# Kernel optimization log

Hardware: AMD Instinct MI355X
Metric: run time of the kernel (lower is better)

The kernel has to match this reference:

```python
import jax, jax.numpy as jnp
import numpy as np

B = 32768          # batch (replay-buffer minibatch)
OBS, ACT = 17, 6   # HalfCheetah-style dims
IN = OBS + ACT
H = 256            # hidden width hard-coded in the module
N = 10             # num_q_nets


def setup_inputs() -> dict:
    key = jax.random.key(0)
    ks = jax.random.split(key, 8)
    # PyTorch Linear default init: U(-1/sqrt(fan_in), 1/sqrt(fan_in)); scale randn similarly.
    s1, s2, s3 = 1.0 / np.sqrt(IN), 1.0 / np.sqrt(H), 1.0 / np.sqrt(H)
    return {
        "state": jax.random.normal(ks[0], (B, OBS), dtype=jnp.float32),
        "action": jax.random.uniform(ks[1], (B, ACT), dtype=jnp.float32, minval=-1.0, maxval=1.0),
        "W1": jax.random.normal(ks[2], (N, IN, H), dtype=jnp.float32) * s1,
        "b1": jax.random.normal(ks[3], (N, H), dtype=jnp.float32) * s1,
        "W2": jax.random.normal(ks[4], (N, H, H), dtype=jnp.float32) * s2,
        "b2": jax.random.normal(ks[5], (N, H), dtype=jnp.float32) * s2,
        "W3": jax.random.normal(ks[6], (N, H, 1), dtype=jnp.float32) * s3,
        "b3": jax.random.normal(ks[7], (N, 1), dtype=jnp.float32) * s3,
    }


def reference(state, action, W1, b1, W2, b2, W3, b3):
    # x: [B, OBS+ACT]
    x = jnp.concatenate([state, action], axis=1)
    # batched-over-ensemble GEMMs; n=ensemble member, b=batch
    h1 = jax.nn.relu(jnp.einsum("bi,nih->nbh", x, W1) + b1[:, None, :])   # [N,B,H]
    h2 = jax.nn.relu(jnp.einsum("nbh,nho->nbo", h1, W2) + b2[:, None, :])  # [N,B,H]
    out = jnp.einsum("nbh,nho->nbo", h2, W3) + b3[:, None, :]              # [N,B,1]
    return out
```

## Files before the change

kernel.cpp:

```cpp
#include <hip/hip_runtime.h>
#include <hip/hip_bf16.h>


typedef __attribute__((ext_vector_type(8))) short bf16x8;
typedef __attribute__((ext_vector_type(4))) float f32x4;

#define B_TOTAL 32768
#define NQ 10
#define HDIM 256
#define BT 64

#define W1P_ELEMS (NQ * 16 * 64 * 8)
#define W2P_ELEMS (NQ * 8 * 16 * 64 * 8)

__device__ __forceinline__ unsigned short f2bf(float f) {
  unsigned int u = __float_as_uint(f);
  u = u + 0x7FFFu + ((u >> 16) & 1u);
  return (unsigned short)(u >> 16);
}

__device__ __forceinline__ unsigned int pk2bf(float a, float b) {
  union { __hip_bfloat162 h; unsigned int u; } cv;
  cv.h = __float22bfloat162_rn(make_float2(a, b));
  return cv.u;
}

__global__ void pack_w_kernel(const float* __restrict__ W1,
                              const float* __restrict__ W2,
                              unsigned short* __restrict__ w1p,
                              unsigned short* __restrict__ w2p) {
  int t = blockIdx.x * 256 + threadIdx.x;
  const int NW1 = NQ * 16 * 64;
  if (t < NW1) {
    int u = t;
    int lane = u & 63, mt = (u >> 6) & 15, n = u >> 10;
    int m = lane & 15, q = lane >> 4;
    int outc = mt * 16 + m;
    unsigned short v[8];
#pragma unroll
    for (int j = 0; j < 8; j++) {
      int k = q * 8 + j;
      v[j] = (k < 23) ? f2bf(W1[(n * 23 + k) * 256 + outc]) : (unsigned short)0;
    }
    *(uint4*)&w1p[(size_t)u * 8] = *(const uint4*)v;
  } else {
    int u = t - NW1;
    int lane = u & 63, mt = (u >> 6) & 15, kt = (u >> 10) & 7, n = u >> 13;
    int m = lane & 15, q = lane >> 4;
    int outc = mt * 16 + m;
    unsigned short v[8];
#pragma unroll
    for (int j = 0; j < 8; j++) {
      int h = kt * 32 + q * 8 + j;
      v[j] = f2bf(W2[((size_t)(n * 256 + h)) * 256 + outc]);
    }
    *(uint4*)&w2p[(size_t)u * 8] = *(const uint4*)v;
  }
}

__global__ __launch_bounds__(256, 4) void fused_ensemble_kernel(
    const float* __restrict__ state,
    const float* __restrict__ action,
    const unsigned short* __restrict__ w1p,
    const float* __restrict__ b1,
    const unsigned short* __restrict__ w2p,
    const float* __restrict__ b2,
    const float* __restrict__ W3,
    const float* __restrict__ b3,
    float* __restrict__ out) {
  __shared__ __align__(16) unsigned short hs[32 * BT * 8];
  __shared__ __align__(16) unsigned short xs[BT * 32];
  __shared__ float red[4 * 64];

  const int tid = threadIdx.x;
  const int lane = tid & 63;
  const int w = tid >> 6;
  const int m = lane & 15;
  const int q = lane >> 4;

  const int n = blockIdx.x >> 9;
  const int row0 = (blockIdx.x & 511) * BT;

  f32x4 acc[4][4];

  bf16x8 af1[4];
#pragma unroll
  for (int mt = 0; mt < 4; mt++)
    af1[mt] = *(const bf16x8*)(w1p + (((size_t)n * 16 + w * 4 + mt) * 64 + lane) * 8);
  float4 b1v[4];
#pragma unroll
  for (int mt = 0; mt < 4; mt++)
    b1v[mt] = *(const float4*)&b1[n * HDIM + (w * 4 + mt) * 16 + q * 4];

  {
    int r = tid >> 2, seg = tid & 3;
    int row = row0 + r;
    unsigned short v[8];
    if (seg < 2) {
      const float* sp = state + (size_t)row * 17 + seg * 8;
#pragma unroll
      for (int j = 0; j < 8; j++) v[j] = f2bf(sp[j]);
    } else if (seg == 2) {
      v[0] = f2bf(state[(size_t)row * 17 + 16]);
      const float* ap = action + (size_t)row * 6;
#pragma unroll
      for (int j = 0; j < 6; j++) v[1 + j] = f2bf(ap[j]);
      v[7] = 0;
    } else {
#pragma unroll
      for (int j = 0; j < 8; j++) v[j] = 0;
    }
    *(uint4*)&xs[(size_t)r * 32 + seg * 8] = *(const uint4*)v;
  }
  __syncthreads();

  {
    bf16x8 bfr[4];
#pragma unroll
    for (int nt = 0; nt < 4; nt++)
      bfr[nt] = *(const bf16x8*)&xs[(size_t)(nt * 16 + m) * 32 + q * 8];
#pragma unroll
    for (int mt = 0; mt < 4; mt++) {
      float4 bv = b1v[mt];
      f32x4 bi = (f32x4){bv.x, bv.y, bv.z, bv.w};
#pragma unroll
      for (int nt = 0; nt < 4; nt++) acc[mt][nt] = bi;
    }
    __builtin_amdgcn_s_setprio(1);
#pragma unroll
    for (int nt = 0; nt < 4; nt++)
#pragma unroll
      for (int mt = 0; mt < 4; mt++)
        acc[mt][nt] = __builtin_amdgcn_mfma_f32_16x16x32_bf16(af1[mt], bfr[nt], acc[mt][nt], 0, 0, 0);
    __builtin_amdgcn_s_setprio(0);
  }

#pragma unroll
  for (int mt = 0; mt < 4; mt++) {
    int kq = w * 8 + mt * 2 + (q >> 1);
    int joff = (q & 1) * 4;
#pragma unroll
    for (int nt = 0; nt < 4; nt++) {
      int col = nt * 16 + m;
      f32x4 a = acc[mt][nt];
      uint2 wv;
      wv.x = pk2bf(fmaxf(a[0], 0.f), fmaxf(a[1], 0.f));
      wv.y = pk2bf(fmaxf(a[2], 0.f), fmaxf(a[3], 0.f));
      *(uint2*)&hs[((size_t)kq * BT + col) * 8 + joff] = wv;
    }
  }

  const unsigned short* w2n = w2p + (size_t)n * (8 * 16 * 64 * 8);
  bf16x8 acur[4], anxt[4];
#pragma unroll
  for (int mt = 0; mt < 4; mt++)
    acur[mt] = *(const bf16x8*)(w2n + (((size_t)w * 4 + mt) * 64 + lane) * 8);
  float4 b2v[4];
#pragma unroll
  for (int mt = 0; mt < 4; mt++)
    b2v[mt] = *(const float4*)&b2[n * HDIM + (w * 4 + mt) * 16 + q * 4];
  __syncthreads();

  {
#pragma unroll
    for (int mt = 0; mt < 4; mt++) {
      float4 bv = b2v[mt];
      f32x4 bi = (f32x4){bv.x, bv.y, bv.z, bv.w};
#pragma unroll
      for (int nt = 0; nt < 4; nt++) acc[mt][nt] = bi;
    }
#pragma unroll
    for (int kt = 0; kt < 8; kt++) {
      if (kt < 7) {
#pragma unroll
        for (int mt = 0; mt < 4; mt++)
          anxt[mt] = *(const bf16x8*)(w2n + (((size_t)(kt + 1) * 16 + w * 4 + mt) * 64 + lane) * 8);
      }
      bf16x8 bfr[4];
#pragma unroll
      for (int nt = 0; nt < 4; nt++)
        bfr[nt] = *(const bf16x8*)&hs[(((size_t)kt * 4 + q) * BT + nt * 16 + m) * 8];
      __builtin_amdgcn_s_setprio(1);
#pragma unroll
      for (int nt = 0; nt < 4; nt++)
#pragma unroll
        for (int mt = 0; mt < 4; mt++)
          acc[mt][nt] = __builtin_amdgcn_mfma_f32_16x16x32_bf16(acur[mt], bfr[nt], acc[mt][nt], 0, 0, 0);
      __builtin_amdgcn_s_setprio(0);
#pragma unroll
      for (int mt = 0; mt < 4; mt++) acur[mt] = anxt[mt];
    }
  }

  {
    float4 w3v[4];
#pragma unroll
    for (int mt = 0; mt < 4; mt++)
      w3v[mt] = *(const float4*)&W3[n * HDIM + (w * 4 + mt) * 16 + q * 4];
    float p[4];
#pragma unroll
    for (int nt = 0; nt < 4; nt++) {
      float s = 0.f;
#pragma unroll
      for (int mt = 0; mt < 4; mt++) {
        f32x4 a = acc[mt][nt];
        float4 wv = w3v[mt];
        s = fmaf(fmaxf(a[0], 0.f), wv.x, s);
        s = fmaf(fmaxf(a[1], 0.f), wv.y, s);
        s = fmaf(fmaxf(a[2], 0.f), wv.z, s);
        s = fmaf(fmaxf(a[3], 0.f), wv.w, s);
      }
      s += __shfl_xor(s, 16, 64);
      s += __shfl_xor(s, 32, 64);
      p[nt] = s;
    }
    if (q == 0) {
#pragma unroll
      for (int nt = 0; nt < 4; nt++) red[w * 64 + nt * 16 + m] = p[nt];
    }
    __syncthreads();
    if (tid < BT) {
      float s = b3[n];
#pragma unroll
      for (int c = 0; c < 4; c++) s += red[c * 64 + tid];
      out[(size_t)n * B_TOTAL + row0 + tid] = s;
    }
  }
}

extern "C" void kernel_launch(void* const* d_in, const int* in_sizes, int n_in,
                              void* d_out, int out_size, void* d_ws, size_t ws_size,
                              hipStream_t stream) {
  const float* state  = (const float*)d_in[0];
  const float* action = (const float*)d_in[1];
  const float* W1 = (const float*)d_in[2];
  const float* b1 = (const float*)d_in[3];
  const float* W2 = (const float*)d_in[4];
  const float* b2 = (const float*)d_in[5];
  const float* W3 = (const float*)d_in[6];
  const float* b3 = (const float*)d_in[7];
  float* out = (float*)d_out;

  unsigned short* w1p = (unsigned short*)d_ws;
  unsigned short* w2p = (unsigned short*)((char*)d_ws + (size_t)W1P_ELEMS * 2);

  pack_w_kernel<<<360, 256, 0, stream>>>(W1, W2, w1p, w2p);
  fused_ensemble_kernel<<<NQ * (B_TOTAL / BT), 256, 0, stream>>>(
      state, action, w1p, b1, w2p, b2, W3, b3, out);
}
```

Baseline: 119.7 us.

## Switch GEMMs to 32x32x16 MFMA tiles and fold b1 into W1 padding

Replaces the 16x16x32 bf16 MFMA tiling with 32x32x16 MFMA instructions, repacking W1/W2 fragments and the LDS layouts of the input and hidden activations to match the new operand layout. Layer-1 bias is folded into the weight matrix by putting b1 in the padded K slot and setting the matching input element to 1.0, so the bias load and accumulator init go away. The larger MFMA tile issues fewer instructions and reuses operands more per instruction. It also changes the accumulator register layout and the shuffle reduction, which could affect register pressure and occupancy.

```diff
diff --git a/kernel.cpp b/kernel.cpp
--- a/kernel.cpp
+++ b/kernel.cpp
@@ -3,15 +3,15 @@
 
 
 typedef __attribute__((ext_vector_type(8))) short bf16x8;
-typedef __attribute__((ext_vector_type(4))) float f32x4;
+typedef __attribute__((ext_vector_type(16))) float f32x16;
 
 #define B_TOTAL 32768
 #define NQ 10
 #define HDIM 256
 #define BT 64
 
-#define W1P_ELEMS (NQ * 16 * 64 * 8)
-#define W2P_ELEMS (NQ * 8 * 16 * 64 * 8)
+#define W1P_ELEMS (NQ * 2 * 8 * 64 * 8)
+#define W2P_ELEMS (NQ * 8 * 2 * 8 * 64 * 8)
 
 __device__ __forceinline__ unsigned short f2bf(float f) {
   unsigned int u = __float_as_uint(f);
@@ -26,34 +26,34 @@
 }
 
 __global__ void pack_w_kernel(const float* __restrict__ W1,
+                              const float* __restrict__ b1,
                               const float* __restrict__ W2,
                               unsigned short* __restrict__ w1p,
                               unsigned short* __restrict__ w2p) {
   int t = blockIdx.x * 256 + threadIdx.x;
-  const int NW1 = NQ * 16 * 64;
+  const int NW1 = NQ * 2 * 8 * 64;
   if (t < NW1) {
     int u = t;
-    int lane = u & 63, mt = (u >> 6) & 15, n = u >> 10;
-    int m = lane & 15, q = lane >> 4;
-    int outc = mt * 16 + m;
+    int lane = u & 63, mtile = (u >> 6) & 7, ks = (u >> 9) & 1, n = u >> 10;
+    int outc = mtile * 32 + (lane & 31);
+    int kbase = ks * 16 + (lane >> 5) * 8;
     unsigned short v[8];
 #pragma unroll
     for (int j = 0; j < 8; j++) {
-      int k = q * 8 + j;
-      v[j] = (k < 23) ? f2bf(W1[(n * 23 + k) * 256 + outc]) : (unsigned short)0;
+      int k = kbase + j;
+      v[j] = (k < 23) ? f2bf(W1[(n * 23 + k) * 256 + outc])
+           : (k == 23) ? f2bf(b1[n * 256 + outc]) : (unsigned short)0;
     }
     *(uint4*)&w1p[(size_t)u * 8] = *(const uint4*)v;
   } else {
     int u = t - NW1;
-    int lane = u & 63, mt = (u >> 6) & 15, kt = (u >> 10) & 7, n = u >> 13;
-    int m = lane & 15, q = lane >> 4;
-    int outc = mt * 16 + m;
+    int lane = u & 63, mtile = (u >> 6) & 7, ks = (u >> 9) & 1, kt = (u >> 10) & 7, n = u >> 13;
+    int outc = mtile * 32 + (lane & 31);
+    int kbase = kt * 32 + ks * 16 + (lane >> 5) * 8;
     unsigned short v[8];
 #pragma unroll
-    for (int j = 0; j < 8; j++) {
-      int h = kt * 32 + q * 8 + j;
-      v[j] = f2bf(W2[((size_t)(n * 256 + h)) * 256 + outc]);
-    }
+    for (int j = 0; j < 8; j++)
+      v[j] = f2bf(W2[((size_t)(n * 256 + kbase + j)) * 256 + outc]);
     *(uint4*)&w2p[(size_t)u * 8] = *(const uint4*)v;
   }
 }
@@ -62,35 +62,32 @@
     const float* __restrict__ state,
     const float* __restrict__ action,
     const unsigned short* __restrict__ w1p,
-    const float* __restrict__ b1,
     const unsigned short* __restrict__ w2p,
     const float* __restrict__ b2,
     const float* __restrict__ W3,
     const float* __restrict__ b3,
     float* __restrict__ out) {
-  __shared__ __align__(16) unsigned short hs[32 * BT * 8];
-  __shared__ __align__(16) unsigned short xs[BT * 32];
+  __shared__ __align__(16) unsigned short hs[32 * 64 * 8];
+  __shared__ __align__(16) unsigned short xs[4 * 64 * 8];
   __shared__ float red[4 * 64];
 
   const int tid = threadIdx.x;
   const int lane = tid & 63;
   const int w = tid >> 6;
-  const int m = lane & 15;
-  const int q = lane >> 4;
+  const int c = lane & 31;
+  const int hi = lane >> 5;
 
   const int n = blockIdx.x >> 9;
   const int row0 = (blockIdx.x & 511) * BT;
 
-  f32x4 acc[4][4];
-
-  bf16x8 af1[4];
-#pragma unroll
-  for (int mt = 0; mt < 4; mt++)
-    af1[mt] = *(const bf16x8*)(w1p + (((size_t)n * 16 + w * 4 + mt) * 64 + lane) * 8);
-  float4 b1v[4];
-#pragma unroll
-  for (int mt = 0; mt < 4; mt++)
-    b1v[mt] = *(const float4*)&b1[n * HDIM + (w * 4 + mt) * 16 + q * 4];
+  f32x16 acc[2][2];
+
+  bf16x8 af1[2][2];
+#pragma unroll
+  for (int ks = 0; ks < 2; ks++)
+#pragma unroll
+    for (int mt = 0; mt < 2; mt++)
+      af1[ks][mt] = *(const bf16x8*)(w1p + ((((size_t)n * 2 + ks) * 8 + w * 2 + mt) * 64 + lane) * 8);
 
   {
     int r = tid >> 2, seg = tid & 3;
@@ -105,124 +102,150 @@
       const float* ap = action + (size_t)row * 6;
 #pragma unroll
       for (int j = 0; j < 6; j++) v[1 + j] = f2bf(ap[j]);
-      v[7] = 0;
+      v[7] = 0x3F80;
     } else {
 #pragma unroll
       for (int j = 0; j < 8; j++) v[j] = 0;
     }
-    *(uint4*)&xs[(size_t)r * 32 + seg * 8] = *(const uint4*)v;
+    *(uint4*)&xs[((size_t)seg * 64 + r) * 8] = *(const uint4*)v;
   }
   __syncthreads();
 
   {
-    bf16x8 bfr[4];
-#pragma unroll
-    for (int nt = 0; nt < 4; nt++)
-      bfr[nt] = *(const bf16x8*)&xs[(size_t)(nt * 16 + m) * 32 + q * 8];
-#pragma unroll
-    for (int mt = 0; mt < 4; mt++) {
-      float4 bv = b1v[mt];
-      f32x4 bi = (f32x4){bv.x, bv.y, bv.z, bv.w};
-#pragma unroll
-      for (int nt = 0; nt < 4; nt++) acc[mt][nt] = bi;
-    }
+    bf16x8 bfr[2][2];
+#pragma unroll
+    for (int ks = 0; ks < 2; ks++)
+#pragma unroll
+      for (int nt = 0; nt < 2; nt++)
+        bfr[ks][nt] = *(const bf16x8*)&xs[(((size_t)ks * 2 + hi) * 64 + nt * 32 + c) * 8];
+    const f32x16 zz = {0.f,0.f,0.f,0.f,0.f,0.f,0.f,0.f,0.f,0.f,0.f,0.f,0.f,0.f,0.f,0.f};
+#pragma unroll
+    for (int mt = 0; mt < 2; mt++)
+#pragma unroll
+      for (int nt = 0; nt < 2; nt++) acc[mt][nt] = zz;
     __builtin_amdgcn_s_setprio(1);
 #pragma unroll
-    for (int nt = 0; nt < 4; nt++)
-#pragma unroll
-      for (int mt = 0; mt < 4; mt++)
-        acc[mt][nt] = __builtin_amdgcn_mfma_f32_16x16x32_bf16(af1[mt], bfr[nt], acc[mt][nt], 0, 0, 0);
+    for (int ks = 0; ks < 2; ks++)
+#pragma unroll
+      for (int nt = 0; nt < 2; nt++)
+#pragma unroll
+        for (int mt = 0; mt < 2; mt++)
+          acc[mt][nt] = __builtin_amdgcn_mfma_f32_32x32x16_bf16(af1[ks][mt], bfr[ks][nt],
+                                                                acc[mt][nt], 0, 0, 0);
     __builtin_amdgcn_s_setprio(0);
   }
 
 #pragma unroll
-  for (int mt = 0; mt < 4; mt++) {
-    int kq = w * 8 + mt * 2 + (q >> 1);
-    int joff = (q & 1) * 4;
-#pragma unroll
-    for (int nt = 0; nt < 4; nt++) {
-      int col = nt * 16 + m;
-      f32x4 a = acc[mt][nt];
-      uint2 wv;
-      wv.x = pk2bf(fmaxf(a[0], 0.f), fmaxf(a[1], 0.f));
-      wv.y = pk2bf(fmaxf(a[2], 0.f), fmaxf(a[3], 0.f));
-      *(uint2*)&hs[((size_t)kq * BT + col) * 8 + joff] = wv;
-    }
-  }
-
-  const unsigned short* w2n = w2p + (size_t)n * (8 * 16 * 64 * 8);
-  bf16x8 acur[4], anxt[4];
-#pragma unroll
-  for (int mt = 0; mt < 4; mt++)
-    acur[mt] = *(const bf16x8*)(w2n + (((size_t)w * 4 + mt) * 64 + lane) * 8);
-  float4 b2v[4];
-#pragma unroll
-  for (int mt = 0; mt < 4; mt++)
-    b2v[mt] = *(const float4*)&b2[n * HDIM + (w * 4 + mt) * 16 + q * 4];
+  for (int mt = 0; mt < 2; mt++)
+#pragma unroll
+    for (int nt = 0; nt < 2; nt++) {
+      f32x16 a = acc[mt][nt];
+#pragma unroll
+      for (int g = 0; g < 4; g++) {
+        uint2 wv;
+        wv.x = pk2bf(fmaxf(a[4 * g + 0], 0.f), fmaxf(a[4 * g + 1], 0.f));
+        wv.y = pk2bf(fmaxf(a[4 * g + 2], 0.f), fmaxf(a[4 * g + 3], 0.f));
+        *(uint2*)&hs[(((size_t)w * 8 + mt * 4 + g) * 64 + nt * 32 + c) * 8 + hi * 4] = wv;
+      }
+    }
+
+  const unsigned short* w2n = w2p + (size_t)n * 65536;
+  bf16x8 acur[2][2], anxt[2][2];
+#pragma unroll
+  for (int ks = 0; ks < 2; ks++)
+#pragma unroll
+    for (int mt = 0; mt < 2; mt++)
+      acur[ks][mt] = *(const bf16x8*)(w2n + (((size_t)ks * 8 + w * 2 + mt) * 64 + lane) * 8);
   __syncthreads();
 
   {
-#pragma unroll
-    for (int mt = 0; mt < 4; mt++) {
-      float4 bv = b2v[mt];
-      f32x4 bi = (f32x4){bv.x, bv.y, bv.z, bv.w};
-#pragma unroll
-      for (int nt = 0; nt < 4; nt++) acc[mt][nt] = bi;
+    float4 b2g[2][4];
+#pragma unroll
+    for (int mt = 0; mt < 2; mt++)
+#pragma unroll
+      for (int g = 0; g < 4; g++)
+        b2g[mt][g] = *(const float4*)&b2[n * HDIM + w * 64 + mt * 32 + g * 8 + hi * 4];
+#pragma unroll
+    for (int mt = 0; mt < 2; mt++) {
+      f32x16 bi;
+#pragma unroll
+      for (int g = 0; g < 4; g++) {
+        bi[4 * g + 0] = b2g[mt][g].x;
+        bi[4 * g + 1] = b2g[mt][g].y;
+        bi[4 * g + 2] = b2g[mt][g].z;
+        bi[4 * g + 3] = b2g[mt][g].w;
+      }
+      acc[mt][0] = bi;
+      acc[mt][1] = bi;
     }
 #pragma unroll
     for (int kt = 0; kt < 8; kt++) {
       if (kt < 7) {
 #pragma unroll
-        for (int mt = 0; mt < 4; mt++)
-          anxt[mt] = *(const bf16x8*)(w2n + (((size_t)(kt + 1) * 16 + w * 4 + mt) * 64 + lane) * 8);
-      }
-      bf16x8 bfr[4];
-#pragma unroll
-      for (int nt = 0; nt < 4; nt++)
-        bfr[nt] = *(const bf16x8*)&hs[(((size_t)kt * 4 + q) * BT + nt * 16 + m) * 8];
+        for (int ks = 0; ks < 2; ks++)
+#pragma unroll
+          for (int mt = 0; mt < 2; mt++)
+            anxt[ks][mt] = *(const bf16x8*)(
+                w2n + ((((size_t)(kt + 1) * 2 + ks) * 8 + w * 2 + mt) * 64 + lane) * 8);
+      }
+      bf16x8 bfr[2][2];
+#pragma unroll
+      for (int ks = 0; ks < 2; ks++)
+#pragma unroll
+        for (int nt = 0; nt < 2; nt++)
+          bfr[ks][nt] = *(const bf16x8*)&hs[(((size_t)kt * 4 + ks * 2 + hi) * 64 + nt * 32 + c) * 8];
       __builtin_amdgcn_s_setprio(1);
 #pragma unroll
-      for (int nt = 0; nt < 4; nt++)
-#pragma unroll
-        for (int mt = 0; mt < 4; mt++)
-          acc[mt][nt] = __builtin_amdgcn_mfma_f32_16x16x32_bf16(acur[mt], bfr[nt], acc[mt][nt], 0, 0, 0);
+      for (int ks = 0; ks < 2; ks++)
+#pragma unroll
+        for (int nt = 0; nt < 2; nt++)
+#pragma unroll
+          for (int mt = 0; mt < 2; mt++)
+            acc[mt][nt] = __builtin_amdgcn_mfma_f32_32x32x16_bf16(acur[ks][mt], bfr[ks][nt],
+                                                                  acc[mt][nt], 0, 0, 0);
       __builtin_amdgcn_s_setprio(0);
 #pragma unroll
-      for (int mt = 0; mt < 4; mt++) acur[mt] = anxt[mt];
-    }
-  }
-
-  {
-    float4 w3v[4];
-#pragma unroll
-    for (int mt = 0; mt < 4; mt++)
-      w3v[mt] = *(const float4*)&W3[n * HDIM + (w * 4 + mt) * 16 + q * 4];
-    float p[4];
-#pragma unroll
-    for (int nt = 0; nt < 4; nt++) {
+      for (int ks = 0; ks < 2; ks++)
+#pragma unroll
+        for (int mt = 0; mt < 2; mt++) acur[ks][mt] = anxt[ks][mt];
+    }
+  }
+
+  {
+    float4 w3g[2][4];
+#pragma unroll
+    for (int mt = 0; mt < 2; mt++)
+#pragma unroll
+      for (int g = 0; g < 4; g++)
+        w3g[mt][g] = *(const float4*)&W3[n * HDIM + w * 64 + mt * 32 + g * 8 + hi * 4];
+    float p[2];
+#pragma unroll
+    for (int nt = 0; nt < 2; nt++) {
       float s = 0.f;
 #pragma unroll
-      for (int mt = 0; mt < 4; mt++) {
-        f32x4 a = acc[mt][nt];
-        float4 wv = w3v[mt];
-        s = fmaf(fmaxf(a[0], 0.f), wv.x, s);
-        s = fmaf(fmaxf(a[1], 0.f), wv.y, s);
-        s = fmaf(fmaxf(a[2], 0.f), wv.z, s);
-        s = fmaf(fmaxf(a[3], 0.f), wv.w, s);
-      }
-      s += __shfl_xor(s, 16, 64);
+      for (int mt = 0; mt < 2; mt++) {
+        f32x16 a = acc[mt][nt];
+#pragma unroll
+        for (int g = 0; g < 4; g++) {
+          float4 wv = w3g[mt][g];
+          s = fmaf(fmaxf(a[4 * g + 0], 0.f), wv.x, s);
+          s = fmaf(fmaxf(a[4 * g + 1], 0.f), wv.y, s);
+          s = fmaf(fmaxf(a[4 * g + 2], 0.f), wv.z, s);
+          s = fmaf(fmaxf(a[4 * g + 3], 0.f), wv.w, s);
+        }
+      }
       s += __shfl_xor(s, 32, 64);
       p[nt] = s;
     }
-    if (q == 0) {
-#pragma unroll
-      for (int nt = 0; nt < 4; nt++) red[w * 64 + nt * 16 + m] = p[nt];
+    if (hi == 0) {
+      red[w * 64 + c] = p[0];
+      red[w * 64 + 32 + c] = p[1];
     }
     __syncthreads();
     if (tid < BT) {
       float s = b3[n];
 #pragma unroll
-      for (int c = 0; c < 4; c++) s += red[c * 64 + tid];
+      for (int cw = 0; cw < 4; cw++) s += red[cw * 64 + tid];
       out[(size_t)n * B_TOTAL + row0 + tid] = s;
     }
   }
@@ -244,7 +267,7 @@
   unsigned short* w1p = (unsigned short*)d_ws;
   unsigned short* w2p = (unsigned short*)((char*)d_ws + (size_t)W1P_ELEMS * 2);
 
-  pack_w_kernel<<<360, 256, 0, stream>>>(W1, W2, w1p, w2p);
+  pack_w_kernel<<<360, 256, 0, stream>>>(W1, b1, W2, w1p, w2p);
   fused_ensemble_kernel<<<NQ * (B_TOTAL / BT), 256, 0, stream>>>(
-      state, action, w1p, b1, w2p, b2, W3, b3, out);
-}
+      state, action, w1p, w2p, b2, W3, b3, out);
+}
```

Result: slower. 128.0 us (+6.9%).
